# Kernel optimization log

Measured on AMD Instinct MI355X. Metric: run time of the kernel, lower is better.

Reference implementation:

```python
import jax, jax.numpy as jnp
import numpy as np

B, NSV, NTRK, K, H = 512, 128, 512, 8, 16


def setup_inputs() -> dict:
    key = jax.random.key(0)
    ks = jax.random.split(key, 12)
    p = lambda k, shp: (jax.random.normal(k, shp, dtype=jnp.float32) * 0.1)
    return {
        "x_sv": jax.random.normal(ks[0], (B * NSV, 2), dtype=jnp.float32),
        "x_trk": jax.random.normal(ks[1], (B * NTRK, 8), dtype=jnp.float32),
        "batch_sv": jnp.repeat(jnp.arange(B, dtype=jnp.int32), NSV),
        "batch_trk": jnp.repeat(jnp.arange(B, dtype=jnp.int32), NTRK),
        # sv_encode: Linear(2,16) -> ELU -> Linear(16,16)
        "W1s": p(ks[2], (2, H)), "b1s": jnp.zeros((H,), jnp.float32),
        "W2s": p(ks[3], (H, H)), "b2s": jnp.zeros((H,), jnp.float32),
        # trk_encode: Linear(8,16) -> ELU -> Linear(16,16)
        "W1t": p(ks[4], (8, H)), "b1t": jnp.zeros((H,), jnp.float32),
        "W2t": p(ks[5], (H, H)), "b2t": jnp.zeros((H,), jnp.float32),
        # edge MLP: Linear(2*16, 16)
        "We": p(ks[6], (2 * H, H)), "be": jnp.zeros((H,), jnp.float32),
        # output head: Linear(16, 1)
        "Wo": p(ks[7], (H, 1)), "bo": jnp.zeros((1,), jnp.float32),
    }


def reference(x_sv, x_trk, batch_sv, batch_trk,
              W1s, b1s, W2s, b2s, W1t, b1t, W2t, b2t, We, be, Wo, bo):
    # Node encoders
    sv = jax.nn.elu(x_sv @ W1s + b1s) @ W2s + b2s      # [Nsv, H]
    trk = jax.nn.elu(x_trk @ W1t + b1t) @ W2t + b2t    # [Ntrk, H]

    # Regular batching: reshape to per-event blocks (batch_sv/batch_trk are
    # contiguous repeats of arange(B) with NSV / NTRK nodes per event).
    svb = sv.reshape(B, NSV, H)      # [B, S, H]
    trkb = trk.reshape(B, NTRK, H)   # [B, T, H]

    # kNN in encoded space: squared L2 distance per event, k nearest SVs per track
    t_sq = jnp.sum(trkb * trkb, -1)[:, :, None]          # [B, T, 1]
    s_sq = jnp.sum(svb * svb, -1)[:, None, :]            # [B, 1, S]
    dots = jnp.einsum("bth,bsh->bts", trkb, svb)         # [B, T, S]
    d2 = t_sq + s_sq - 2.0 * dots                        # [B, T, S]
    _, idx = jax.lax.top_k(-d2, K)                       # [B, T, K] indices into S

    # Gather neighbor SV features: [B, T, K, H]
    nbr = jax.vmap(lambda s, i: s[i])(svb, idx)

    # EdgeConv message: nn(cat[x_i, x_j - x_i]), x_i = track (target), x_j = SV
    ti = trkb[:, :, None, :]                                    # [B, T, 1, H]
    msg_in = jnp.concatenate(
        [jnp.broadcast_to(ti, nbr.shape), nbr - ti], axis=-1)   # [B, T, K, 2H]
    msg = msg_in @ We + be                                      # [B, T, K, H]
    feats = jnp.max(msg, axis=2).reshape(B * NTRK, H)           # max aggregation

    # Output head + per-event average pool (avg_pool_x with cluster == batch)
    out = jax.nn.sigmoid(feats @ Wo + bo)                       # [Ntrk, 1]
    sums = jax.ops.segment_sum(out, batch_trk, num_segments=B)  # [B, 1]
    cnts = jax.ops.segment_sum(jnp.ones_like(out), batch_trk, num_segments=B)
    pooled = sums / cnts                                        # [B, 1]
    batch_out = jnp.arange(B, dtype=jnp.int32)
    return pooled, batch_out
```

## Files before the change

### kernel.cpp

```cpp
#include <hip/hip_runtime.h>
#include <cmath>

#define BB   512
#define NSV  128
#define NTRK 512
#define KK   8
#define HH   16
#define TPB  512
#define TST  36
#define SST  36
#define PSTR 20

typedef float    f32x4  __attribute__((ext_vector_type(4)));
typedef short    bf16x8 __attribute__((ext_vector_type(8)));
typedef unsigned u32x4  __attribute__((ext_vector_type(4)));

__device__ __forceinline__ float elu_f(float x) {
    float e = __builtin_amdgcn_exp2f(x * 1.44269504088896341f) - 1.0f;
    return x > 0.0f ? x : e;
}
__device__ __forceinline__ unsigned umin_u(unsigned a, unsigned b) { return a < b ? a : b; }
__device__ __forceinline__ unsigned umax_u(unsigned a, unsigned b) { return a > b ? a : b; }
__device__ __forceinline__ unsigned med3u(unsigned a, unsigned b, unsigned c) {
    unsigned d;
    asm("v_med3_u32 %0, %1, %2, %3" : "=v"(d) : "v"(a), "v"(b), "v"(c));
    return d;
}
__device__ __forceinline__ bf16x8 mk_bf8(uint2 a, uint2 b) {
    u32x4 u; u.x = a.x; u.y = a.y; u.z = b.x; u.w = b.y;
    return __builtin_bit_cast(bf16x8, u);
}
__device__ __forceinline__ float uasf(unsigned u) { return __uint_as_float(u); }

__global__ __launch_bounds__(TPB, 4) void fused_all(
    const float* __restrict__ x_sv, const float* __restrict__ x_trk,
    const float* __restrict__ W1s, const float* __restrict__ b1s,
    const float* __restrict__ W2s, const float* __restrict__ b2s,
    const float* __restrict__ W1t, const float* __restrict__ b1t,
    const float* __restrict__ W2t, const float* __restrict__ b2t,
    const float* __restrict__ We,  const float* __restrict__ be,
    const float* __restrict__ Wo,  const float* __restrict__ bo,
    float* __restrict__ out)
{
    __shared__ __align__(16) short Tsh[NTRK * TST];
    __shared__ __align__(16) short Ssh[NSV * SST];
    __shared__ __align__(16) float hsqS[NSV];
    __shared__ __align__(16) float proj[NSV][PSTR];
    __shared__ __align__(16) float ucS[HH + 1];
    __shared__ __align__(16) float WoS[HH];
    __shared__ float sred[TPB / 64];

    const int b = blockIdx.x, tid = threadIdx.x;

    {
        const float* xp = x_trk + (size_t)(b * NTRK + tid) * 8;
        float x[8];
        *(float4*)&x[0] = *(const float4*)&xp[0];
        *(float4*)&x[4] = *(const float4*)&xp[4];
        float hb[HH];
        #pragma unroll
        for (int h = 0; h < HH; ++h) {
            float a = b1t[h];
            #pragma unroll
            for (int i = 0; i < 8; ++i) a += x[i] * W1t[i * HH + h];
            hb[h] = elu_f(a);
        }
        float tf[HH], sq = 0.0f;
        #pragma unroll
        for (int h2 = 0; h2 < HH; ++h2) {
            float a = b2t[h2];
            #pragma unroll
            for (int h = 0; h < HH; ++h) a += hb[h] * W2t[h * HH + h2];
            tf[h2] = a;
            sq += a * a;
        }
        unsigned hw[8], lw[8];
        #pragma unroll
        for (int j = 0; j < 8; ++j) {
            float f0 = tf[2 * j], f1 = tf[2 * j + 1];
            unsigned u0 = __float_as_uint(f0) & 0xFFFF0000u;
            unsigned u1 = __float_as_uint(f1) & 0xFFFF0000u;
            hw[j] = (u0 >> 16) | u1;
            float r0 = f0 - uasf(u0);
            float r1 = f1 - uasf(u1);
            lw[j] = (__float_as_uint(r0) >> 16) | (__float_as_uint(r1) & 0xFFFF0000u);
        }
        unsigned* tr = (unsigned*)&Tsh[tid * TST];
        *(uint2*)(tr + 0)  = make_uint2(hw[0], hw[1]);
        *(uint2*)(tr + 2)  = make_uint2(hw[2], hw[3]);
        *(uint2*)(tr + 4)  = make_uint2(hw[4], hw[5]);
        *(uint2*)(tr + 6)  = make_uint2(hw[6], hw[7]);
        *(uint2*)(tr + 8)  = make_uint2(lw[0], lw[1]);
        *(uint2*)(tr + 10) = make_uint2(lw[2], lw[3]);
        *(uint2*)(tr + 12) = make_uint2(lw[4], lw[5]);
        *(uint2*)(tr + 14) = make_uint2(lw[6], lw[7]);
        ((float*)tr)[16] = 0.5f * sq;
    }

    if (tid < NSV) {
        const float* xp = x_sv + (size_t)(b * NSV + tid) * 2;
        float x0 = xp[0], x1 = xp[1];
        float hb[HH];
        #pragma unroll
        for (int h = 0; h < HH; ++h)
            hb[h] = elu_f(x0 * W1s[h] + x1 * W1s[HH + h] + b1s[h]);
        float o[HH], sq = 0.0f;
        #pragma unroll
        for (int h2 = 0; h2 < HH; ++h2) {
            float a = b2s[h2];
            #pragma unroll
            for (int h = 0; h < HH; ++h) a += hb[h] * W2s[h * HH + h2];
            o[h2] = a;
            sq += a * a;
        }
        unsigned hw[8], lw[8];
        #pragma unroll
        for (int j = 0; j < 8; ++j) {
            float f0 = o[2 * j], f1 = o[2 * j + 1];
            unsigned u0 = __float_as_uint(f0) & 0xFFFF0000u;
            unsigned u1 = __float_as_uint(f1) & 0xFFFF0000u;
            hw[j] = (u0 >> 16) | u1;
            float r0 = f0 - uasf(u0);
            float r1 = f1 - uasf(u1);
            lw[j] = (__float_as_uint(r0) >> 16) | (__float_as_uint(r1) & 0xFFFF0000u);
        }
        unsigned* sr = (unsigned*)&Ssh[tid * SST];
        *(uint2*)(sr + 0)  = make_uint2(hw[0], hw[1]);
        *(uint2*)(sr + 2)  = make_uint2(hw[2], hw[3]);
        *(uint2*)(sr + 4)  = make_uint2(hw[4], hw[5]);
        *(uint2*)(sr + 6)  = make_uint2(hw[6], hw[7]);
        *(uint2*)(sr + 8)  = make_uint2(lw[0], lw[1]);
        *(uint2*)(sr + 10) = make_uint2(lw[2], lw[3]);
        *(uint2*)(sr + 12) = make_uint2(lw[4], lw[5]);
        *(uint2*)(sr + 14) = make_uint2(lw[6], lw[7]);
        hsqS[tid] = 0.5f * sq;
        #pragma unroll
        for (int h = 0; h < HH; ++h) {
            float a = 0.0f;
            #pragma unroll
            for (int j = 0; j < HH; ++j) a += o[j] * We[(HH + j) * HH + h];
            proj[tid][h] = a;
        }
    } else if (tid < NSV + HH) {
        int j = tid - NSV;
        float a = 0.0f;
        #pragma unroll
        for (int h = 0; h < HH; ++h)
            a += (We[j * HH + h] - We[(HH + j) * HH + h]) * Wo[h];
        ucS[j] = a;
    } else if (tid < NSV + 2 * HH) {
        int j = tid - NSV - HH;
        WoS[j] = Wo[j];
    } else if (tid == NSV + 2 * HH) {
        float a = bo[0];
        #pragma unroll
        for (int h = 0; h < HH; ++h) a += be[h] * Wo[h];
        ucS[HH] = a;
    }

    __syncthreads();

    float wsum = 0.0f;
    {
        const int lane = tid & 63;
        const int w    = tid >> 6;
        const int c    = lane & 15;
        const int g    = lane >> 4;
        const int g4   = g << 2;
        const int gd   = (g & 1) << 2;

        const unsigned* tp0 = (const unsigned*)&Tsh[((w     ) * 16 + c) * TST];
        const unsigned* tp1 = (const unsigned*)&Tsh[((w +  8) * 16 + c) * TST];
        const unsigned* tp2 = (const unsigned*)&Tsh[((w + 16) * 16 + c) * TST];
        const unsigned* tp3 = (const unsigned*)&Tsh[((w + 24) * 16 + c) * TST];
        bf16x8 bf0 = mk_bf8(*(const uint2*)(tp0 + g * 4), *(const uint2*)(tp0 + g * 4 + 2));
        bf16x8 bf1 = mk_bf8(*(const uint2*)(tp1 + g * 4), *(const uint2*)(tp1 + g * 4 + 2));
        bf16x8 bf2 = mk_bf8(*(const uint2*)(tp2 + g * 4), *(const uint2*)(tp2 + g * 4 + 2));
        bf16x8 bf3 = mk_bf8(*(const uint2*)(tp3 + g * 4), *(const uint2*)(tp3 + g * 4 + 2));
        const float ht0 = ((const float*)tp0)[16];
        const float ht1 = ((const float*)tp1)[16];
        const float ht2 = ((const float*)tp2)[16];
        const float ht3 = ((const float*)tp3)[16];

        unsigned k00=~0u,k01=~0u,k02=~0u,k03=~0u,k04=~0u,k05=~0u,k06=~0u,k07=~0u;
        unsigned k10=~0u,k11=~0u,k12=~0u,k13=~0u,k14=~0u,k15=~0u,k16=~0u,k17=~0u;
        unsigned k20=~0u,k21=~0u,k22=~0u,k23=~0u,k24=~0u,k25=~0u,k26=~0u,k27=~0u;
        unsigned k30=~0u,k31=~0u,k32=~0u,k33=~0u,k34=~0u,k35=~0u,k36=~0u,k37=~0u;

        #define CHAIN(v,K0,K1,K2,K3,K4,K5,K6,K7)                           \
            do {                                                           \
                unsigned nk0 = umin_u(v, K0);                              \
                unsigned nk1 = med3u(v, K0, K1);                           \
                unsigned nk2 = med3u(v, K1, K2);                           \
                unsigned nk3 = med3u(v, K2, K3);                           \
                unsigned nk4 = med3u(v, K3, K4);                           \
                unsigned nk5 = med3u(v, K4, K5);                           \
                unsigned nk6 = med3u(v, K5, K6);                           \
                unsigned nk7 = med3u(v, K6, K7);                           \
                K0 = nk0; K1 = nk1; K2 = nk2; K3 = nk3;                    \
                K4 = nk4; K5 = nk5; K6 = nk6; K7 = nk7;                    \
            } while (0)

        #define CONSUME(T, accv)                                           \
            do {                                                           \
                float e0 = fmaxf((ht##T - accv.x) + hq.x, 0.0f);           \
                float e1 = fmaxf((ht##T - accv.y) + hq.y, 0.0f);           \
                float e2 = fmaxf((ht##T - accv.z) + hq.z, 0.0f);           \
                float e3 = fmaxf((ht##T - accv.w) + hq.w, 0.0f);           \
                unsigned v0 = (__float_as_uint(e0) & 0xFFFFFF80u) | (unsigned)(sbase + 0); \
                CHAIN(v0,k##T##0,k##T##1,k##T##2,k##T##3,k##T##4,k##T##5,k##T##6,k##T##7); \
                unsigned v1 = (__float_as_uint(e1) & 0xFFFFFF80u) | (unsigned)(sbase + 1); \
                CHAIN(v1,k##T##0,k##T##1,k##T##2,k##T##3,k##T##4,k##T##5,k##T##6,k##T##7); \
                unsigned v2 = (__float_as_uint(e2) & 0xFFFFFF80u) | (unsigned)(sbase + 2); \
                CHAIN(v2,k##T##0,k##T##1,k##T##2,k##T##3,k##T##4,k##T##5,k##T##6,k##T##7); \
                unsigned v3 = (__float_as_uint(e3) & 0xFFFFFF80u) | (unsigned)(sbase + 3); \
                CHAIN(v3,k##T##0,k##T##1,k##T##2,k##T##3,k##T##4,k##T##5,k##T##6,k##T##7); \
            } while (0)

        #pragma unroll
        for (int ss = 0; ss < 8; ++ss) {
            const unsigned* sp = (const unsigned*)&Ssh[(ss * 16 + c) * SST];
            bf16x8 ah = mk_bf8(*(const uint2*)(sp + gd), *(const uint2*)(sp + gd + 2));
            bf16x8 al = mk_bf8(*(const uint2*)(sp + 8 + gd), *(const uint2*)(sp + 8 + gd + 2));
            f32x4 hq = *(const f32x4*)&hsqS[ss * 16 + g4];
            const int sbase = ss * 16 + g4;
            f32x4 a0 = {0.f, 0.f, 0.f, 0.f}, a1 = a0, a2 = a0, a3 = a0;
            a0 = __builtin_amdgcn_mfma_f32_16x16x32_bf16(ah, bf0, a0, 0, 0, 0);
            a1 = __builtin_amdgcn_mfma_f32_16x16x32_bf16(ah, bf1, a1, 0, 0, 0);
            a2 = __builtin_amdgcn_mfma_f32_16x16x32_bf16(ah, bf2, a2, 0, 0, 0);
            a3 = __builtin_amdgcn_mfma_f32_16x16x32_bf16(ah, bf3, a3, 0, 0, 0);
            a0 = __builtin_amdgcn_mfma_f32_16x16x32_bf16(al, bf0, a0, 0, 0, 0);
            a1 = __builtin_amdgcn_mfma_f32_16x16x32_bf16(al, bf1, a1, 0, 0, 0);
            a2 = __builtin_amdgcn_mfma_f32_16x16x32_bf16(al, bf2, a2, 0, 0, 0);
            a3 = __builtin_amdgcn_mfma_f32_16x16x32_bf16(al, bf3, a3, 0, 0, 0);
            CONSUME(0, a0);
            CONSUME(1, a1);
            CONSUME(2, a2);
            CONSUME(3, a3);
        }
        #undef CONSUME
        #undef CHAIN

        #define CEX(a, bq) do { unsigned _lo = umin_u(a, bq); unsigned _hi = umax_u(a, bq); a = _lo; bq = _hi; } while (0)
        #define MERGE_EPI(T, TP)                                           \
            do {                                                           \
                unsigned m0 = umin_u(k##T##0, __shfl_xor(k##T##7, 32, 64));\
                unsigned m1 = umin_u(k##T##1, __shfl_xor(k##T##6, 32, 64));\
                unsigned m2 = umin_u(k##T##2, __shfl_xor(k##T##5, 32, 64));\
                unsigned m3 = umin_u(k##T##3, __shfl_xor(k##T##4, 32, 64));\
                unsigned m4 = umin_u(k##T##4, __shfl_xor(k##T##3, 32, 64));\
                unsigned m5 = umin_u(k##T##5, __shfl_xor(k##T##2, 32, 64));\
                unsigned m6 = umin_u(k##T##6, __shfl_xor(k##T##1, 32, 64));\
                unsigned m7 = umin_u(k##T##7, __shfl_xor(k##T##0, 32, 64));\
                CEX(m0, m4); CEX(m1, m5); CEX(m2, m6); CEX(m3, m7);        \
                CEX(m0, m2); CEX(m1, m3); CEX(m4, m6); CEX(m5, m7);        \
                CEX(m0, m1); CEX(m2, m3); CEX(m4, m5); CEX(m6, m7);        \
                unsigned f0 = umin_u(m0, __shfl_xor(m7, 16, 64));          \
                unsigned f1 = umin_u(m1, __shfl_xor(m6, 16, 64));          \
                unsigned f2 = umin_u(m2, __shfl_xor(m5, 16, 64));          \
                unsigned f3 = umin_u(m3, __shfl_xor(m4, 16, 64));          \
                unsigned f4 = umin_u(m4, __shfl_xor(m3, 16, 64));          \
                unsigned f5 = umin_u(m5, __shfl_xor(m2, 16, 64));          \
                unsigned f6 = umin_u(m6, __shfl_xor(m1, 16, 64));          \
                unsigned f7 = umin_u(m7, __shfl_xor(m0, 16, 64));          \
                uint2 th = *(const uint2*)((TP) + 2 * g);                  \
                uint2 tl = *(const uint2*)((TP) + 8 + 2 * g);              \
                float tfa = uasf(th.x << 16)         + uasf(tl.x << 16);   \
                float tfb = uasf(th.x & 0xFFFF0000u) + uasf(tl.x & 0xFFFF0000u); \
                float tfc = uasf(th.y << 16)         + uasf(tl.y << 16);   \
                float tfd = uasf(th.y & 0xFFFF0000u) + uasf(tl.y & 0xFFFF0000u); \
                f32x4 uc4 = *(const f32x4*)&ucS[g4];                       \
                f32x4 wo4 = *(const f32x4*)&WoS[g4];                       \
                float part = (g == 0) ? ucS[HH] : 0.0f;                    \
                part = fmaf(tfa, uc4.x, part);                             \
                part = fmaf(tfb, uc4.y, part);                             \
                part = fmaf(tfc, uc4.z, part);                             \
                part = fmaf(tfd, uc4.w, part);                             \
                f32x4 mx = {-INFINITY, -INFINITY, -INFINITY, -INFINITY};   \
                mx = __builtin_elementwise_max(mx, *(const f32x4*)&proj[f0 & 127u][g4]); \
                mx = __builtin_elementwise_max(mx, *(const f32x4*)&proj[f1 & 127u][g4]); \
                mx = __builtin_elementwise_max(mx, *(const f32x4*)&proj[f2 & 127u][g4]); \
                mx = __builtin_elementwise_max(mx, *(const f32x4*)&proj[f3 & 127u][g4]); \
                mx = __builtin_elementwise_max(mx, *(const f32x4*)&proj[f4 & 127u][g4]); \
                mx = __builtin_elementwise_max(mx, *(const f32x4*)&proj[f5 & 127u][g4]); \
                mx = __builtin_elementwise_max(mx, *(const f32x4*)&proj[f6 & 127u][g4]); \
                mx = __builtin_elementwise_max(mx, *(const f32x4*)&proj[f7 & 127u][g4]); \
                part = fmaf(mx.x, wo4.x, part);                            \
                part = fmaf(mx.y, wo4.y, part);                            \
                part = fmaf(mx.z, wo4.z, part);                            \
                part = fmaf(mx.w, wo4.w, part);                            \
                part += __shfl_xor(part, 16, 64);                          \
                part += __shfl_xor(part, 32, 64);                          \
                float sg = __builtin_amdgcn_rcpf(1.0f + __builtin_amdgcn_exp2f(part * -1.44269504088896341f)); \
                if (g == 0) wsum += sg;                                    \
            } while (0)

        MERGE_EPI(0, tp0);
        MERGE_EPI(1, tp1);
        MERGE_EPI(2, tp2);
        MERGE_EPI(3, tp3);
        #undef MERGE_EPI
        #undef CEX
    }

    #pragma unroll
    for (int off = 32; off > 0; off >>= 1)
        wsum += __shfl_down(wsum, off, 64);
    if ((tid & 63) == 0) sred[tid >> 6] = wsum;
    __syncthreads();
    if (tid == 0) {
        float tot = 0.0f;
        #pragma unroll
        for (int w2 = 0; w2 < TPB / 64; ++w2) tot += sred[w2];
        out[b]      = tot * (1.0f / NTRK);
        out[BB + b] = (float)b;
    }
}

extern "C" void kernel_launch(void* const* d_in, const int* in_sizes, int n_in,
                              void* d_out, int out_size, void* d_ws, size_t ws_size,
                              hipStream_t stream) {
    const float* x_sv  = (const float*)d_in[0];
    const float* x_trk = (const float*)d_in[1];
    const float* W1s = (const float*)d_in[4];
    const float* b1s = (const float*)d_in[5];
    const float* W2s = (const float*)d_in[6];
    const float* b2s = (const float*)d_in[7];
    const float* W1t = (const float*)d_in[8];
    const float* b1t = (const float*)d_in[9];
    const float* W2t = (const float*)d_in[10];
    const float* b2t = (const float*)d_in[11];
    const float* We  = (const float*)d_in[12];
    const float* be  = (const float*)d_in[13];
    const float* Wo  = (const float*)d_in[14];
    const float* bo  = (const float*)d_in[15];
    float* out = (float*)d_out;

    fused_all<<<BB, TPB, 0, stream>>>(x_sv, x_trk,
                                      W1s, b1s, W2s, b2s,
                                      W1t, b1t, W2t, b2t,
                                      We, be, Wo, bo,
                                      out);
}
```

Baseline: 123.6 us.

## Double block size to 1024 threads, halving track tiles per wave

Raises the block to 1024 threads (16 waves), so each wave handles 2 track tiles of 16 instead of 4. This cuts per-thread top-k register state and MFMA chains and adds wave-level parallelism per event. Encoder work is remapped so that threads 0-511 encode tracks and threads 512+ encode SVs and constants, which lets SV encoding run concurrently with track encoding. The trade-off is more SV-operand LDS reloads per block (each wave reads all SVs for fewer tracks) and a tighter register budget per thread to fit the larger block.

```diff
diff --git a/kernel.cpp b/kernel.cpp
--- a/kernel.cpp
+++ b/kernel.cpp
@@ -6,7 +6,7 @@
 #define NTRK 512
 #define KK   8
 #define HH   16
-#define TPB  512
+#define TPB  1024
 #define TST  36
 #define SST  36
 #define PSTR 20
@@ -32,7 +32,7 @@
 }
 __device__ __forceinline__ float uasf(unsigned u) { return __uint_as_float(u); }
 
-__global__ __launch_bounds__(TPB, 4) void fused_all(
+__global__ __launch_bounds__(TPB, 8) void fused_all(
     const float* __restrict__ x_sv, const float* __restrict__ x_trk,
     const float* __restrict__ W1s, const float* __restrict__ b1s,
     const float* __restrict__ W2s, const float* __restrict__ b2s,
@@ -52,7 +52,7 @@
 
     const int b = blockIdx.x, tid = threadIdx.x;
 
-    {
+    if (tid < NTRK) {
         const float* xp = x_trk + (size_t)(b * NTRK + tid) * 8;
         float x[8];
         *(float4*)&x[0] = *(const float4*)&xp[0];
@@ -95,10 +95,9 @@
         *(uint2*)(tr + 12) = make_uint2(lw[4], lw[5]);
         *(uint2*)(tr + 14) = make_uint2(lw[6], lw[7]);
         ((float*)tr)[16] = 0.5f * sq;
-    }
-
-    if (tid < NSV) {
-        const float* xp = x_sv + (size_t)(b * NSV + tid) * 2;
+    } else if (tid < NTRK + NSV) {
+        const int s = tid - NTRK;
+        const float* xp = x_sv + (size_t)(b * NSV + s) * 2;
         float x0 = xp[0], x1 = xp[1];
         float hb[HH];
         #pragma unroll
@@ -124,7 +123,7 @@
             float r1 = f1 - uasf(u1);
             lw[j] = (__float_as_uint(r0) >> 16) | (__float_as_uint(r1) & 0xFFFF0000u);
         }
-        unsigned* sr = (unsigned*)&Ssh[tid * SST];
+        unsigned* sr = (unsigned*)&Ssh[s * SST];
         *(uint2*)(sr + 0)  = make_uint2(hw[0], hw[1]);
         *(uint2*)(sr + 2)  = make_uint2(hw[2], hw[3]);
         *(uint2*)(sr + 4)  = make_uint2(hw[4], hw[5]);
@@ -133,25 +132,25 @@
         *(uint2*)(sr + 10) = make_uint2(lw[2], lw[3]);
         *(uint2*)(sr + 12) = make_uint2(lw[4], lw[5]);
         *(uint2*)(sr + 14) = make_uint2(lw[6], lw[7]);
-        hsqS[tid] = 0.5f * sq;
+        hsqS[s] = 0.5f * sq;
         #pragma unroll
         for (int h = 0; h < HH; ++h) {
             float a = 0.0f;
             #pragma unroll
             for (int j = 0; j < HH; ++j) a += o[j] * We[(HH + j) * HH + h];
-            proj[tid][h] = a;
-        }
-    } else if (tid < NSV + HH) {
-        int j = tid - NSV;
+            proj[s][h] = a;
+        }
+    } else if (tid < NTRK + NSV + HH) {
+        int j = tid - NTRK - NSV;
         float a = 0.0f;
         #pragma unroll
         for (int h = 0; h < HH; ++h)
             a += (We[j * HH + h] - We[(HH + j) * HH + h]) * Wo[h];
         ucS[j] = a;
-    } else if (tid < NSV + 2 * HH) {
-        int j = tid - NSV - HH;
+    } else if (tid < NTRK + NSV + 2 * HH) {
+        int j = tid - NTRK - NSV - HH;
         WoS[j] = Wo[j];
-    } else if (tid == NSV + 2 * HH) {
+    } else if (tid == NTRK + NSV + 2 * HH) {
         float a = bo[0];
         #pragma unroll
         for (int h = 0; h < HH; ++h) a += be[h] * Wo[h];
@@ -170,22 +169,14 @@
         const int gd   = (g & 1) << 2;
 
         const unsigned* tp0 = (const unsigned*)&Tsh[((w     ) * 16 + c) * TST];
-        const unsigned* tp1 = (const unsigned*)&Tsh[((w +  8) * 16 + c) * TST];
-        const unsigned* tp2 = (const unsigned*)&Tsh[((w + 16) * 16 + c) * TST];
-        const unsigned* tp3 = (const unsigned*)&Tsh[((w + 24) * 16 + c) * TST];
+        const unsigned* tp1 = (const unsigned*)&Tsh[((w + 16) * 16 + c) * TST];
         bf16x8 bf0 = mk_bf8(*(const uint2*)(tp0 + g * 4), *(const uint2*)(tp0 + g * 4 + 2));
         bf16x8 bf1 = mk_bf8(*(const uint2*)(tp1 + g * 4), *(const uint2*)(tp1 + g * 4 + 2));
-        bf16x8 bf2 = mk_bf8(*(const uint2*)(tp2 + g * 4), *(const uint2*)(tp2 + g * 4 + 2));
-        bf16x8 bf3 = mk_bf8(*(const uint2*)(tp3 + g * 4), *(const uint2*)(tp3 + g * 4 + 2));
         const float ht0 = ((const float*)tp0)[16];
         const float ht1 = ((const float*)tp1)[16];
-        const float ht2 = ((const float*)tp2)[16];
-        const float ht3 = ((const float*)tp3)[16];
 
         unsigned k00=~0u,k01=~0u,k02=~0u,k03=~0u,k04=~0u,k05=~0u,k06=~0u,k07=~0u;
         unsigned k10=~0u,k11=~0u,k12=~0u,k13=~0u,k14=~0u,k15=~0u,k16=~0u,k17=~0u;
-        unsigned k20=~0u,k21=~0u,k22=~0u,k23=~0u,k24=~0u,k25=~0u,k26=~0u,k27=~0u;
-        unsigned k30=~0u,k31=~0u,k32=~0u,k33=~0u,k34=~0u,k35=~0u,k36=~0u,k37=~0u;
 
         #define CHAIN(v,K0,K1,K2,K3,K4,K5,K6,K7)                           \
             do {                                                           \
@@ -224,19 +215,13 @@
             bf16x8 al = mk_bf8(*(const uint2*)(sp + 8 + gd), *(const uint2*)(sp + 8 + gd + 2));
             f32x4 hq = *(const f32x4*)&hsqS[ss * 16 + g4];
             const int sbase = ss * 16 + g4;
-            f32x4 a0 = {0.f, 0.f, 0.f, 0.f}, a1 = a0, a2 = a0, a3 = a0;
+            f32x4 a0 = {0.f, 0.f, 0.f, 0.f}, a1 = a0;
             a0 = __builtin_amdgcn_mfma_f32_16x16x32_bf16(ah, bf0, a0, 0, 0, 0);
             a1 = __builtin_amdgcn_mfma_f32_16x16x32_bf16(ah, bf1, a1, 0, 0, 0);
-            a2 = __builtin_amdgcn_mfma_f32_16x16x32_bf16(ah, bf2, a2, 0, 0, 0);
-            a3 = __builtin_amdgcn_mfma_f32_16x16x32_bf16(ah, bf3, a3, 0, 0, 0);
             a0 = __builtin_amdgcn_mfma_f32_16x16x32_bf16(al, bf0, a0, 0, 0, 0);
             a1 = __builtin_amdgcn_mfma_f32_16x16x32_bf16(al, bf1, a1, 0, 0, 0);
-            a2 = __builtin_amdgcn_mfma_f32_16x16x32_bf16(al, bf2, a2, 0, 0, 0);
-            a3 = __builtin_amdgcn_mfma_f32_16x16x32_bf16(al, bf3, a3, 0, 0, 0);
             CONSUME(0, a0);
             CONSUME(1, a1);
-            CONSUME(2, a2);
-            CONSUME(3, a3);
         }
         #undef CONSUME
         #undef CHAIN
@@ -297,8 +282,6 @@
 
         MERGE_EPI(0, tp0);
         MERGE_EPI(1, tp1);
-        MERGE_EPI(2, tp2);
-        MERGE_EPI(3, tp3);
         #undef MERGE_EPI
         #undef CEX
     }
```

Measured after the change: 115.2 us. 6.8% less time.
